# Optimization experiments

Hardware: AMD Instinct MI355X
Metric: run time of the kernel (lower is better)

## Reference

```python
import jax, jax.numpy as jnp
import numpy as np

B, S, D = 2, 2048, 1024
H = 16
DH = D // H  # 64

def setup_inputs() -> dict:
    key = jax.random.key(0)
    ks = jax.random.split(key, 7)
    sc = 1.0 / np.sqrt(DH)
    return {
        "sequences": jax.random.normal(ks[0], (B, S, D), dtype=jnp.float32),
        "Wq": jax.random.normal(ks[1], (H, DH, DH), dtype=jnp.float32) * sc,
        "bq": jax.random.normal(ks[2], (H, DH), dtype=jnp.float32) * 0.02,
        "Wk": jax.random.normal(ks[3], (H, DH, DH), dtype=jnp.float32) * sc,
        "bk": jax.random.normal(ks[4], (H, DH), dtype=jnp.float32) * 0.02,
        "Wv": jax.random.normal(ks[5], (H, DH, DH), dtype=jnp.float32) * sc,
        "bv": jax.random.normal(ks[6], (H, DH), dtype=jnp.float32) * 0.02,
    }

def reference(sequences, Wq, bq, Wk, bk, Wv, bv):
    b, s, _ = sequences.shape
    x = sequences.reshape(b, s, H, DH)  # [B,S,H,Dh]
    # torch Linear: y = x @ W^T + b; W is [out,in] => einsum contracts input dim d
    q = jnp.einsum("bshd,hed->bshe", x, Wq) + bq  # [B,S,H,Dh]
    k = jnp.einsum("bshd,hed->bshe", x, Wk) + bk
    v = jnp.einsum("bshd,hed->bshe", x, Wv) + bv
    scores = jnp.einsum("bshd,bthd->bhst", q, k) / jnp.sqrt(jnp.float32(DH))
    attn = jax.nn.softmax(scores, axis=-1)  # [B,H,S,S]
    out = jnp.einsum("bhst,bthd->bshd", attn, v)  # [B,S,H,Dh]
    return out.reshape(b, s, H * DH)
```

## Files before the change

### kernel.cpp

```cpp
#include <hip/hip_runtime.h>

typedef unsigned short u16;
typedef unsigned int   u32;
typedef __bf16 bf16x8 __attribute__((ext_vector_type(8)));
typedef float  f32x4  __attribute__((ext_vector_type(4)));
typedef float  f32x16 __attribute__((ext_vector_type(16)));
typedef u16    u16x4  __attribute__((ext_vector_type(4)));
typedef u32    u32x4  __attribute__((ext_vector_type(4)));

#define HH   16
#define DHH  64
#define SEQL 2048
#define NB   2
#define BHN  (NB * HH)
#define SCLF 0.1803368801111204f

static __device__ __forceinline__ u16 f2bf(float f) {
    return __builtin_bit_cast(u16, (__bf16)f);
}
static __device__ __forceinline__ u32 pack2(float a, float b) {
    return (u32)f2bf(a) | ((u32)f2bf(b) << 16);
}
static __device__ __forceinline__ void plswap(u32 &a, u32 &b) {
    asm volatile("v_permlane32_swap_b32 %0, %1" : "+v"(a), "+v"(b));
}

static __device__ __forceinline__ void gload_lds16(const void* g, void* l) {
    __builtin_amdgcn_global_load_lds(
        (const __attribute__((address_space(1))) unsigned int*)g,
        (__attribute__((address_space(3))) unsigned int*)l, 16, 0, 0);
}

__global__ __launch_bounds__(256) void wconv_kernel(
    const float* __restrict__ Wq, const float* __restrict__ Wk,
    const float* __restrict__ Wv, u16* __restrict__ Wb)
{
    const int m = blockIdx.y;
    const float* W = (m == 0) ? Wq : (m == 1) ? Wk : Wv;
    const float s = (m == 0) ? SCLF : 1.0f;
    const int i = (blockIdx.x * 256 + threadIdx.x) * 4;
    float4 v = *reinterpret_cast<const float4*>(W + i);
    u16x4 o = { f2bf(v.x * s), f2bf(v.y * s), f2bf(v.z * s), f2bf(v.w * s) };
    *reinterpret_cast<u16x4*>(Wb + (size_t)m * 65536 + i) = o;
}

__global__ __launch_bounds__(256) void qkv_kernel(
    const float* __restrict__ x, const u16* __restrict__ Wb,
    const float* __restrict__ bq, const float* __restrict__ bk,
    const float* __restrict__ bv,
    u16* __restrict__ Qws, u16* __restrict__ Kws, u16* __restrict__ Vtws)
{
    const int h   = blockIdx.y;
    const int r0  = blockIdx.x * 64;
    const int tid = threadIdx.x;
    const int w   = tid >> 6;
    const int l   = tid & 63;
    const int c   = l & 15;
    const int g   = l >> 4;

    __shared__ u16 vt[64 * 72];

    bf16x8 xa[2];
    {
        const float* xp = x + (size_t)(r0 + w * 16 + c) * 1024 + h * 64 + g * 8;
        #pragma unroll
        for (int kh = 0; kh < 2; ++kh) {
            float4 lo = *reinterpret_cast<const float4*>(xp + kh * 32);
            float4 hi = *reinterpret_cast<const float4*>(xp + kh * 32 + 4);
            bf16x8 f;
            f[0]=(__bf16)lo.x; f[1]=(__bf16)lo.y; f[2]=(__bf16)lo.z; f[3]=(__bf16)lo.w;
            f[4]=(__bf16)hi.x; f[5]=(__bf16)hi.y; f[6]=(__bf16)hi.z; f[7]=(__bf16)hi.w;
            xa[kh] = f;
        }
    }

    const int b      = r0 >> 11;
    const int s_base = r0 & (SEQL - 1);
    const int bh     = b * HH + h;

    const float* bs[3] = {bq + h * 64, bk + h * 64, bv + h * 64};

    #pragma unroll
    for (int m = 0; m < 3; ++m) {
        const u16*   W    = Wb + (size_t)m * 65536 + h * 4096;
        const float* bias = bs[m];
        const float  bscl = (m == 0) ? SCLF : 1.0f;
        f32x4 acc[4];
        #pragma unroll
        for (int ct = 0; ct < 4; ++ct) {
            acc[ct][0] = 0.f; acc[ct][1] = 0.f; acc[ct][2] = 0.f; acc[ct][3] = 0.f;
        }
        #pragma unroll
        for (int kh = 0; kh < 2; ++kh) {
            #pragma unroll
            for (int ct = 0; ct < 4; ++ct) {
                bf16x8 wf = *reinterpret_cast<const bf16x8*>(
                    W + (ct * 16 + c) * 64 + kh * 32 + g * 8);
                acc[ct] = __builtin_amdgcn_mfma_f32_16x16x32_bf16(xa[kh], wf, acc[ct], 0, 0, 0);
            }
        }
        if (m < 2) {
            if (m == 1) __syncthreads();
            #pragma unroll
            for (int ct = 0; ct < 4; ++ct) {
                float bb = bias[ct * 16 + c] * bscl;
                #pragma unroll
                for (int r = 0; r < 4; ++r)
                    vt[(w * 16 + g * 4 + r) * 72 + ct * 16 + c] = f2bf(acc[ct][r] + bb);
            }
            __syncthreads();
            {
                const int d  = tid >> 2;
                const int s0 = (tid & 3) * 16;
                u16* outp = (m == 0 ? Qws : Kws) +
                            ((size_t)bh * SEQL + s_base + d) * 64 + s0;
                uint4 v0 = *reinterpret_cast<const uint4*>(&vt[d * 72 + s0]);
                uint4 v1 = *reinterpret_cast<const uint4*>(&vt[d * 72 + s0 + 8]);
                *reinterpret_cast<uint4*>(outp)     = v0;
                *reinterpret_cast<uint4*>(outp + 8) = v1;
            }
        } else {
            __syncthreads();
            #pragma unroll
            for (int ct = 0; ct < 4; ++ct) {
                float bb = bias[ct * 16 + c];
                u16x4 pb;
                #pragma unroll
                for (int r = 0; r < 4; ++r)
                    pb[r] = f2bf(acc[ct][r] + bb);
                *reinterpret_cast<u16x4*>(&vt[(ct * 16 + c) * 72 + w * 16 + g * 4]) = pb;
            }
            __syncthreads();
            {
                const int d  = tid >> 2;
                const int s0 = (tid & 3) * 16;
                u16* vp = Vtws + ((size_t)bh * 64 + d) * SEQL + s_base + s0;
                uint4 v0 = *reinterpret_cast<const uint4*>(&vt[d * 72 + s0]);
                uint4 v1 = *reinterpret_cast<const uint4*>(&vt[d * 72 + s0 + 8]);
                *reinterpret_cast<uint4*>(vp)     = v0;
                *reinterpret_cast<uint4*>(vp + 8) = v1;
            }
        }
    }
}

__global__ __launch_bounds__(256, 2) void attn_kernel(
    const u16* __restrict__ Qws, const u16* __restrict__ Kws,
    const u16* __restrict__ Vtws, float* __restrict__ out)
{
    const int p     = blockIdx.x;
    const int lid   = (p & 7) * 64 + (p >> 3);
    const int qtile = lid & 15;
    const int bh    = lid >> 4;
    const int b     = bh >> 4;
    const int h     = bh & 15;

    const int tid = threadIdx.x;
    const int w   = tid >> 6;
    const int l   = tid & 63;
    const int lq  = l & 31;
    const int hi  = l >> 5;
    const int q0  = qtile * 128 + w * 32;

    __shared__ u16 k_lds[2][64 * 64];
    __shared__ u16 v_lds[2][64 * 64];

    const u16* Kb = Kws  + (size_t)bh * SEQL * 64;
    const u16* Vb = Vtws + (size_t)bh * 64 * SEQL;

    const int rs8 = l >> 3;
    const int sx  = (l & 7) ^ rs8;

    #define STAGE(bb, k0)                                                     \
    {   _Pragma("unroll")                                                     \
        for (int a = 0; a < 2; ++a) {                                         \
            const int rbase = w * 16 + a * 8;                                 \
            const int r     = rbase + rs8;                                    \
            gload_lds16(Kb + (size_t)((k0) + r) * 64 + sx * 8,                \
                        &k_lds[bb][rbase * 64]);                              \
            gload_lds16(Vb + (size_t)r * SEQL + (k0) + sx * 8,                \
                        &v_lds[bb][rbase * 64]);                              \
        }                                                                     \
    }

    bf16x8 qf[4];
    #pragma unroll
    for (int s = 0; s < 4; ++s)
        qf[s] = *reinterpret_cast<const bf16x8*>(
            Qws + ((size_t)bh * SEQL + q0 + lq) * 64 + s * 16 + hi * 8);

    f32x16 zero16;
    #pragma unroll
    for (int j = 0; j < 16; ++j) zero16[j] = 0.f;

    f32x16 acc[2];
    acc[0] = zero16; acc[1] = zero16;
    float mrow = -1e30f;
    float lrow = 0.f;

    int koff[4];
    #pragma unroll
    for (int s = 0; s < 4; ++s) koff[s] = ((s * 2 + hi) ^ (lq & 7)) * 16;

    bf16x8 vfA[2][4], vfB[2][4];
    bf16x8 pfA[4], pfB[4];

    STAGE(0, 0);
    __syncthreads();

    auto body = [&](bf16x8 (&vfC)[2][4], bf16x8 (&pfC)[4],
                    bf16x8 (&vfP)[2][4], bf16x8 (&pfP)[4],
                    int t, bool has_prev) {
        const int cur = t & 1;
        if (t + 1 < SEQL / 64) STAGE(cur ^ 1, (t + 1) * 64);

        const char* kb = reinterpret_cast<const char*>(&k_lds[cur][0]);
        bf16x8 kf0[4], kf1[4];
        #pragma unroll
        for (int s = 0; s < 4; ++s) {
            kf0[s] = *reinterpret_cast<const bf16x8*>(kb + lq * 128 + koff[s]);
            kf1[s] = *reinterpret_cast<const bf16x8*>(kb + (32 + lq) * 128 + koff[s]);
        }

        __builtin_amdgcn_s_setprio(1);
        f32x16 st0 = __builtin_amdgcn_mfma_f32_32x32x16_bf16(kf0[0], qf[0], zero16, 0, 0, 0);
        f32x16 st1 = __builtin_amdgcn_mfma_f32_32x32x16_bf16(kf1[0], qf[0], zero16, 0, 0, 0);
        #pragma unroll
        for (int s = 1; s < 4; ++s) {
            st0 = __builtin_amdgcn_mfma_f32_32x32x16_bf16(kf0[s], qf[s], st0, 0, 0, 0);
            st1 = __builtin_amdgcn_mfma_f32_32x32x16_bf16(kf1[s], qf[s], st1, 0, 0, 0);
        }
        if (has_prev) {
            #pragma unroll
            for (int s = 0; s < 4; ++s) {
                acc[0] = __builtin_amdgcn_mfma_f32_32x32x16_bf16(vfP[0][s], pfP[s], acc[0], 0, 0, 0);
                acc[1] = __builtin_amdgcn_mfma_f32_32x32x16_bf16(vfP[1][s], pfP[s], acc[1], 0, 0, 0);
            }
        }
        __builtin_amdgcn_s_setprio(0);

        const char* vb = reinterpret_cast<const char*>(&v_lds[cur][0]);
        #pragma unroll
        for (int dt = 0; dt < 2; ++dt)
            #pragma unroll
            for (int s = 0; s < 4; ++s)
                vfC[dt][s] = *reinterpret_cast<const bf16x8*>(vb + (dt * 32 + lq) * 128 + koff[s]);

        float t0 = fmaxf(fmaxf(st0[0], st0[1]),  fmaxf(st0[2], st0[3]));
        float t1 = fmaxf(fmaxf(st0[4], st0[5]),  fmaxf(st0[6], st0[7]));
        float t2 = fmaxf(fmaxf(st0[8], st0[9]),  fmaxf(st0[10], st0[11]));
        float t3 = fmaxf(fmaxf(st0[12], st0[13]), fmaxf(st0[14], st0[15]));
        float t4 = fmaxf(fmaxf(st1[0], st1[1]),  fmaxf(st1[2], st1[3]));
        float t5 = fmaxf(fmaxf(st1[4], st1[5]),  fmaxf(st1[6], st1[7]));
        float t6 = fmaxf(fmaxf(st1[8], st1[9]),  fmaxf(st1[10], st1[11]));
        float t7 = fmaxf(fmaxf(st1[12], st1[13]), fmaxf(st1[14], st1[15]));
        float mx = fmaxf(fmaxf(fmaxf(t0, t1), fmaxf(t2, t3)),
                         fmaxf(fmaxf(t4, t5), fmaxf(t6, t7)));
        mx = fmaxf(mx, __shfl_xor(mx, 32, 64));

        if (!__all(mx <= mrow + 8.f)) {
            const float mn    = fmaxf(mrow, mx);
            const float alpha = __builtin_amdgcn_exp2f(mrow - mn);
            mrow = mn;
            lrow *= alpha;
            #pragma unroll
            for (int j = 0; j < 16; ++j) { acc[0][j] *= alpha; acc[1][j] *= alpha; }
        }

        float rs0 = 0.f, rs1 = 0.f;
        u32 wd[16];
        {
            float pp[16];
            #pragma unroll
            for (int r = 0; r < 16; ++r) {
                pp[r] = __builtin_amdgcn_exp2f(st0[r] - mrow);
                if (r & 1) rs1 += pp[r]; else rs0 += pp[r];
            }
            #pragma unroll
            for (int j = 0; j < 8; ++j) wd[j] = pack2(pp[2 * j], pp[2 * j + 1]);
        }
        {
            float pp[16];
            #pragma unroll
            for (int r = 0; r < 16; ++r) {
                pp[r] = __builtin_amdgcn_exp2f(st1[r] - mrow);
                if (r & 1) rs1 += pp[r]; else rs0 += pp[r];
            }
            #pragma unroll
            for (int j = 0; j < 8; ++j) wd[8 + j] = pack2(pp[2 * j], pp[2 * j + 1]);
        }
        lrow += rs0 + rs1;

        plswap(wd[0],  wd[2]);  plswap(wd[1],  wd[3]);
        plswap(wd[4],  wd[6]);  plswap(wd[5],  wd[7]);
        plswap(wd[8],  wd[10]); plswap(wd[9],  wd[11]);
        plswap(wd[12], wd[14]); plswap(wd[13], wd[15]);

        #pragma unroll
        for (int s = 0; s < 4; ++s) {
            u32x4 tmp = { wd[s * 4 + 0], wd[s * 4 + 1], wd[s * 4 + 2], wd[s * 4 + 3] };
            pfC[s] = __builtin_bit_cast(bf16x8, tmp);
        }

        __syncthreads();
    };

    for (int tt = 0; tt < SEQL / 64; tt += 2) {
        body(vfA, pfA, vfB, pfB, tt,     tt != 0);
        body(vfB, pfB, vfA, pfA, tt + 1, true);
    }

    #pragma unroll
    for (int s = 0; s < 4; ++s) {
        acc[0] = __builtin_amdgcn_mfma_f32_32x32x16_bf16(vfB[0][s], pfB[s], acc[0], 0, 0, 0);
        acc[1] = __builtin_amdgcn_mfma_f32_32x32x16_bf16(vfB[1][s], pfB[s], acc[1], 0, 0, 0);
    }
    const float inv = 1.f / (lrow + __shfl_xor(lrow, 32, 64));

    float* op = out + ((size_t)b * SEQL + q0 + lq) * 1024 + h * 64 + hi * 4;
    #pragma unroll
    for (int dt = 0; dt < 2; ++dt)
        #pragma unroll
        for (int rg = 0; rg < 4; ++rg) {
            float4 o;
            o.x = acc[dt][rg * 4 + 0] * inv;
            o.y = acc[dt][rg * 4 + 1] * inv;
            o.z = acc[dt][rg * 4 + 2] * inv;
            o.w = acc[dt][rg * 4 + 3] * inv;
            *reinterpret_cast<float4*>(op + dt * 32 + rg * 8) = o;
        }
}

extern "C" void kernel_launch(void* const* d_in, const int* in_sizes, int n_in,
                              void* d_out, int out_size, void* d_ws, size_t ws_size,
                              hipStream_t stream) {
    const float* x  = (const float*)d_in[0];
    const float* Wq = (const float*)d_in[1];
    const float* bq = (const float*)d_in[2];
    const float* Wk = (const float*)d_in[3];
    const float* bk = (const float*)d_in[4];
    const float* Wv = (const float*)d_in[5];
    const float* bv = (const float*)d_in[6];
    float* out = (float*)d_out;

    const size_t per = (size_t)BHN * SEQL * 64;
    u16* Qws = (u16*)d_ws;
    u16* Kws = Qws + per;
    u16* Vt  = Kws + per;
    u16* Wb  = Vt  + per;

    wconv_kernel<<<dim3(64, 3), 256, 0, stream>>>(Wq, Wk, Wv, Wb);
    qkv_kernel<<<dim3(64, 16), 256, 0, stream>>>(x, Wb, bq, bk, bv, Qws, Kws, Vt);
    attn_kernel<<<dim3(512), 256, 0, stream>>>(Qws, Kws, Vt, out);
}
```

Before: 84.90 us.

## Double KV tile to 128 keys per stage, halving barriers per sequence

Stages 128 keys of K and V per double-buffered LDS stage instead of 64, and processes each stage as two 64-key sub-iterations with a single barrier at the end. V tiles switch to a 256-byte row stride with a 16-slot XOR swizzle. The aim is fewer __syncthreads and prefetch issues per key, hiding global-to-LDS latency better. The cost is doubled LDS use (64KB per block), which may limit the two-blocks-per-CU occupancy target.

Result: slower. 87.92 us (+3.6%).

```diff
diff --git a/kernel.cpp b/kernel.cpp
--- a/kernel.cpp
+++ b/kernel.cpp
@@ -14,6 +14,8 @@
 #define NB   2
 #define BHN  (NB * HH)
 #define SCLF 0.1803368801111204f
+#define KVB  128
+#define NT   (SEQL / KVB)
 
 static __device__ __forceinline__ u16 f2bf(float f) {
     return __builtin_bit_cast(u16, (__bf16)f);
@@ -162,24 +164,27 @@
     const int hi  = l >> 5;
     const int q0  = qtile * 128 + w * 32;
 
-    __shared__ u16 k_lds[2][64 * 64];
-    __shared__ u16 v_lds[2][64 * 64];
+    __shared__ u16 k_lds[2][KVB * 64];
+    __shared__ u16 v_lds[2][64 * KVB];
 
     const u16* Kb = Kws  + (size_t)bh * SEQL * 64;
     const u16* Vb = Vtws + (size_t)bh * 64 * SEQL;
 
-    const int rs8 = l >> 3;
-    const int sx  = (l & 7) ^ rs8;
-
     #define STAGE(bb, k0)                                                     \
-    {   _Pragma("unroll")                                                     \
-        for (int a = 0; a < 2; ++a) {                                         \
-            const int rbase = w * 16 + a * 8;                                 \
-            const int r     = rbase + rs8;                                    \
-            gload_lds16(Kb + (size_t)((k0) + r) * 64 + sx * 8,                \
+    {   const int rs8 = l >> 3, c8 = l & 7;                                   \
+        _Pragma("unroll")                                                     \
+        for (int a = 0; a < 4; ++a) {                                         \
+            const int rbase = w * 32 + a * 8;                                 \
+            gload_lds16(Kb + (size_t)((k0) + rbase + rs8) * 64 + (c8 ^ rs8) * 8, \
                         &k_lds[bb][rbase * 64]);                              \
-            gload_lds16(Vb + (size_t)r * SEQL + (k0) + sx * 8,                \
-                        &v_lds[bb][rbase * 64]);                              \
+        }                                                                     \
+        const int rs16 = l >> 4, c16 = l & 15;                                \
+        _Pragma("unroll")                                                     \
+        for (int a = 0; a < 4; ++a) {                                         \
+            const int rbase = w * 16 + a * 4;                                 \
+            const int sxv   = c16 ^ ((a * 4 + rs16) & 15);                    \
+            gload_lds16(Vb + (size_t)(rbase + rs16) * SEQL + (k0) + sxv * 8,  \
+                        &v_lds[bb][rbase * KVB]);                             \
         }                                                                     \
     }
 
@@ -208,13 +213,10 @@
     STAGE(0, 0);
     __syncthreads();
 
-    auto body = [&](bf16x8 (&vfC)[2][4], bf16x8 (&pfC)[4],
-                    bf16x8 (&vfP)[2][4], bf16x8 (&pfP)[4],
-                    int t, bool has_prev) {
-        const int cur = t & 1;
-        if (t + 1 < SEQL / 64) STAGE(cur ^ 1, (t + 1) * 64);
-
-        const char* kb = reinterpret_cast<const char*>(&k_lds[cur][0]);
+    auto subbody = [&](bf16x8 (&vfC)[2][4], bf16x8 (&pfC)[4],
+                       bf16x8 (&vfP)[2][4], bf16x8 (&pfP)[4],
+                       int cur, int ks, bool has_prev) {
+        const char* kb = reinterpret_cast<const char*>(&k_lds[cur][0]) + ks * (64 * 128);
         bf16x8 kf0[4], kf1[4];
         #pragma unroll
         for (int s = 0; s < 4; ++s) {
@@ -243,8 +245,11 @@
         #pragma unroll
         for (int dt = 0; dt < 2; ++dt)
             #pragma unroll
-            for (int s = 0; s < 4; ++s)
-                vfC[dt][s] = *reinterpret_cast<const bf16x8*>(vb + (dt * 32 + lq) * 128 + koff[s]);
+            for (int s = 0; s < 4; ++s) {
+                const int slot = (ks * 8 + s * 2 + hi) ^ (lq & 15);
+                vfC[dt][s] = *reinterpret_cast<const bf16x8*>(
+                    vb + (dt * 32 + lq) * 256 + slot * 16);
+            }
 
         float t0 = fmaxf(fmaxf(st0[0], st0[1]),  fmaxf(st0[2], st0[3]));
         float t1 = fmaxf(fmaxf(st0[4], st0[5]),  fmaxf(st0[6], st0[7]));
@@ -301,13 +306,14 @@
             u32x4 tmp = { wd[s * 4 + 0], wd[s * 4 + 1], wd[s * 4 + 2], wd[s * 4 + 3] };
             pfC[s] = __builtin_bit_cast(bf16x8, tmp);
         }
-
+    };
+
+    for (int t = 0; t < NT; ++t) {
+        const int cur = t & 1;
+        if (t + 1 < NT) STAGE(cur ^ 1, (t + 1) * KVB);
+        subbody(vfA, pfA, vfB, pfB, cur, 0, t != 0);
+        subbody(vfB, pfB, vfA, pfA, cur, 1, true);
         __syncthreads();
-    };
-
-    for (int tt = 0; tt < SEQL / 64; tt += 2) {
-        body(vfA, pfA, vfB, pfB, tt,     tt != 0);
-        body(vfB, pfB, vfA, pfA, tt + 1, true);
     }
 
     #pragma unroll
```
